# Kernel optimization log

Hardware: AMD Instinct MI355X
Metric: run time of the kernel (lower is better)

## Reference

```python
import jax, jax.numpy as jnp
import numpy as np

D = 1024      # n_embd
NH = 16       # attention heads
E = 8         # n_experts
K = 2         # k_best
FF = 4 * D    # expert MLP hidden
EPS = 1e-6    # rms_norm_epsilon
TEMP = 1.0    # target_temperature


def setup_inputs() -> dict:
    key = jax.random.key(0)
    ks = jax.random.split(key, 12)
    B, S = 2, 1024
    s = 0.02
    return {
        "x": jax.random.normal(ks[0], (B, S, D), jnp.float32),
        "attn_norm_w": jnp.ones((D,), jnp.float32),
        "wq": jax.random.normal(ks[1], (D, D), jnp.float32) * s,
        "wk": jax.random.normal(ks[2], (D, D), jnp.float32) * s,
        "wv": jax.random.normal(ks[3], (D, D), jnp.float32) * s,
        "wo": jax.random.normal(ks[4], (D, D), jnp.float32) * s,
        "mlp_norm_w": jnp.ones((D,), jnp.float32),
        "router_w": jax.random.normal(ks[5], (D, E), jnp.float32) * s,
        "w1": jax.random.normal(ks[6], (E, D, FF), jnp.float32) * s,
        "b1": jnp.zeros((E, FF), jnp.float32),
        "w2": jax.random.normal(ks[7], (E, FF, D), jnp.float32) * s,
        "b2": jnp.zeros((E, D), jnp.float32),
    }


def _rmsnorm(x, w):
    var = jnp.mean(jnp.square(x), axis=-1, keepdims=True)
    return x * jax.lax.rsqrt(var + EPS) * w


def _attention(x, wq, wk, wv, wo):
    B, S, _ = x.shape
    dh = D // NH
    q = (x @ wq).reshape(B, S, NH, dh)
    k = (x @ wk).reshape(B, S, NH, dh)
    v = (x @ wv).reshape(B, S, NH, dh)
    scores = jnp.einsum("bqhd,bkhd->bhqk", q, k) / jnp.sqrt(jnp.float32(dh))
    causal = jnp.tril(jnp.ones((S, S), bool))  # [S,S]
    scores = jnp.where(causal[None, None], scores, jnp.finfo(scores.dtype).min)
    attn = jax.nn.softmax(scores, axis=-1)
    out = jnp.einsum("bhqk,bkhd->bqhd", attn, v).reshape(B, S, D)
    return out @ wo


def reference(x, attn_norm_w, wq, wk, wv, wo, mlp_norm_w, router_w, w1, b1, w2, b2):
    B, S, _ = x.shape
    # attention sub-block
    x = x + _attention(_rmsnorm(x, attn_norm_w), wq, wk, wv, wo)
    residual = x
    h = _rmsnorm(x, mlp_norm_w)  # [B,S,D]

    # router: temperature softmax + top-k
    logits = h @ router_w / TEMP                      # [B,S,E]
    probs = jax.nn.softmax(logits, axis=-1)
    top_k_scores, top_k_indices = jax.lax.top_k(probs, K)  # [B,S,K]
    onehot = jax.nn.one_hot(top_k_indices, E, dtype=h.dtype)  # [B,S,K,E]
    gates = jnp.einsum("bsk,bske->bse", top_k_scores, onehot)  # [B,S,E]

    # load-balancing loss (Switch-style) + expert counts
    counts = jnp.sum(onehot, axis=(0, 1, 2))          # [E]
    frac = counts / (B * S * K)
    mean_prob = jnp.mean(probs, axis=(0, 1))          # [E]
    balancing_loss = E * jnp.sum(frac * mean_prob)

    # experts: dense dispatch; tokens with zero gate contribute nothing,
    # so this matches the sort/gather/scatter top-k combine exactly.
    pre = jnp.einsum("bsd,edf->ebsf", h, w1) + b1[:, None, None]  # [E,B,S,FF]
    act = jax.nn.gelu(pre)
    y = jnp.einsum("ebsf,efd->ebsd", act, w2) + b2[:, None, None]  # [E,B,S,D]
    moe = jnp.einsum("ebsd,bse->bsd", y, gates)

    out = residual + moe
    return out, balancing_loss, counts
```

## Files before the change

### kernel.cpp

```cpp
#include <hip/hip_runtime.h>

typedef __bf16 bf16;
typedef __bf16 bf16x8 __attribute__((ext_vector_type(8)));
typedef float f32x4 __attribute__((ext_vector_type(4)));

#define D_   1024
#define S_   1024
#define B_   2
#define NTOK 2048
#define FF_  4096
#define NE   8
#define CAP  5120
#define OUTN 2097152

__device__ __forceinline__ float gelu_f(float x) {
    return 0.5f * x * (1.0f + tanhf(0.7978845608028654f * (x + 0.044715f * x * x * x)));
}

__device__ __forceinline__ void gload16(const void* g, void* l) {
    __builtin_amdgcn_global_load_lds((const __attribute__((address_space(1))) unsigned int*)g,
                                     (__attribute__((address_space(3))) unsigned int*)l,
                                     16, 0, 0);
}

__global__ __launch_bounds__(256) void rmsnorm_k(const float* __restrict__ x,
                                                 const float* __restrict__ w,
                                                 float* __restrict__ yf,
                                                 bf16* __restrict__ yhi,
                                                 bf16* __restrict__ ylo) {
    int row = blockIdx.x;
    int t = threadIdx.x;
    const float* xr = x + (size_t)row * D_;
    float4 v = *(const float4*)(xr + t * 4);
    float ss = v.x * v.x + v.y * v.y + v.z * v.z + v.w * v.w;
    for (int off = 32; off; off >>= 1) ss += __shfl_down(ss, off);
    __shared__ float wsum[4];
    if ((t & 63) == 0) wsum[t >> 6] = ss;
    __syncthreads();
    float tot = wsum[0] + wsum[1] + wsum[2] + wsum[3];
    float rr = rsqrtf(tot * (1.0f / D_) + 1e-6f);
    float4 wv = *(const float4*)(w + t * 4);
    float y[4];
    y[0] = v.x * rr * wv.x; y[1] = v.y * rr * wv.y;
    y[2] = v.z * rr * wv.z; y[3] = v.w * rr * wv.w;
    if (yf) *(float4*)(yf + (size_t)row * D_ + t * 4) = *(float4*)y;
    if (yhi) {
#pragma unroll
        for (int i = 0; i < 4; i++) {
            bf16 hi = (bf16)y[i];
            yhi[(size_t)row * D_ + t * 4 + i] = hi;
            if (ylo) ylo[(size_t)row * D_ + t * 4 + i] = (bf16)(y[i] - (float)hi);
        }
    }
}

__global__ __launch_bounds__(256) void trans_split_k(
    const float* __restrict__ w0, const float* __restrict__ w1p,
    const float* __restrict__ w2p, const float* __restrict__ w3,
    bf16* o0h, bf16* o0l, bf16* o1h, bf16* o1l,
    bf16* o2h, bf16* o2l, bf16* o3h, bf16* o3l) {
    int z = blockIdx.z;
    const float* src = (z == 0) ? w0 : (z == 1) ? w1p : (z == 2) ? w2p : w3;
    bf16* dh = (z == 0) ? o0h : (z == 1) ? o1h : (z == 2) ? o2h : o3h;
    bf16* dl = (z == 0) ? o0l : (z == 1) ? o1l : (z == 2) ? o2l : o3l;
    __shared__ float tl[32][33];
    int c0 = blockIdx.x * 32, r0 = blockIdx.y * 32;
    int tx = threadIdx.x & 31, ty = threadIdx.x >> 5;
#pragma unroll
    for (int i = 0; i < 4; i++) {
        int r = ty + i * 8;
        tl[r][tx] = src[(size_t)(r0 + r) * 1024 + c0 + tx];
    }
    __syncthreads();
#pragma unroll
    for (int i = 0; i < 4; i++) {
        int c = ty + i * 8;
        float v = tl[tx][c];
        bf16 hi = (bf16)v;
        dh[(size_t)(c0 + c) * 1024 + r0 + tx] = hi;
        dl[(size_t)(c0 + c) * 1024 + r0 + tx] = (bf16)(v - (float)hi);
    }
}

__global__ __launch_bounds__(256) void transpose_cast_k(const float* __restrict__ in,
                                                        bf16* __restrict__ out,
                                                        int R, int C) {
    __shared__ float tl[32][33];
    size_t base = (size_t)blockIdx.z * R * C;
    const float* src = in + base;
    bf16* dst = out + base;
    int c0 = blockIdx.x * 32, r0 = blockIdx.y * 32;
    int tx = threadIdx.x & 31, tyy = threadIdx.x >> 5;
#pragma unroll
    for (int i = 0; i < 4; i++) {
        int r = tyy + i * 8;
        tl[r][tx] = src[(size_t)(r0 + r) * C + c0 + tx];
    }
    __syncthreads();
#pragma unroll
    for (int i = 0; i < 4; i++) {
        int c = tyy + i * 8;
        dst[(size_t)(c0 + c) * R + r0 + tx] = (bf16)tl[tx][c];
    }
}

#define GLD 40

#define GEMM64_SPLIT_BODY(N0EXPR, EPILOGUE)                                            \
    __shared__ bf16 Ash[64 * GLD], Asl[64 * GLD], Bsh[64 * GLD], Bsl[64 * GLD];        \
    int t = threadIdx.x;                                                               \
    int m0 = blockIdx.x * 64;                                                          \
    int n0 = (N0EXPR);                                                                 \
    int wv = t >> 6, ln = t & 63, l15 = ln & 15, qd = ln >> 4;                         \
    int srow = t >> 2, skc = (t & 3) * 8;                                              \
    f32x4 acc[4];                                                                      \
    _Pragma("unroll") for (int mt = 0; mt < 4; mt++) acc[mt] = (f32x4){0.f,0.f,0.f,0.f}; \
    for (int k0 = 0; k0 < 1024; k0 += 32) {                                            \
        __syncthreads();                                                               \
        *(bf16x8*)&Ash[srow * GLD + skc] = *(const bf16x8*)(Ah + (size_t)(m0 + srow) * 1024 + k0 + skc); \
        *(bf16x8*)&Asl[srow * GLD + skc] = *(const bf16x8*)(Al + (size_t)(m0 + srow) * 1024 + k0 + skc); \
        *(bf16x8*)&Bsh[srow * GLD + skc] = *(const bf16x8*)(Bh + (size_t)(n0 + srow) * 1024 + k0 + skc); \
        *(bf16x8*)&Bsl[srow * GLD + skc] = *(const bf16x8*)(Bl + (size_t)(n0 + srow) * 1024 + k0 + skc); \
        __syncthreads();                                                               \
        bf16x8 ah[4], al[4];                                                           \
        _Pragma("unroll") for (int mt = 0; mt < 4; mt++) {                             \
            ah[mt] = *(const bf16x8*)&Ash[(mt * 16 + l15) * GLD + qd * 8];             \
            al[mt] = *(const bf16x8*)&Asl[(mt * 16 + l15) * GLD + qd * 8];             \
        }                                                                              \
        bf16x8 bh = *(const bf16x8*)&Bsh[(wv * 16 + l15) * GLD + qd * 8];              \
        bf16x8 bl = *(const bf16x8*)&Bsl[(wv * 16 + l15) * GLD + qd * 8];              \
        _Pragma("unroll") for (int mt = 0; mt < 4; mt++) {                             \
            acc[mt] = __builtin_amdgcn_mfma_f32_16x16x32_bf16(ah[mt], bh, acc[mt], 0, 0, 0); \
            acc[mt] = __builtin_amdgcn_mfma_f32_16x16x32_bf16(ah[mt], bl, acc[mt], 0, 0, 0); \
            acc[mt] = __builtin_amdgcn_mfma_f32_16x16x32_bf16(al[mt], bh, acc[mt], 0, 0, 0); \
        }                                                                              \
    }                                                                                  \
    int gnl = wv * 16 + l15;                                                           \
    _Pragma("unroll") for (int mt = 0; mt < 4; mt++)                                   \
        _Pragma("unroll") for (int r = 0; r < 4; r++) {                                \
            int gm = m0 + mt * 16 + qd * 4 + r;                                        \
            float vv = acc[mt][r];                                                     \
            EPILOGUE                                                                   \
        }

__global__ __launch_bounds__(256) void gemm_qkv_k(
    const bf16* __restrict__ Ah, const bf16* __restrict__ Al,
    const bf16* __restrict__ Bqh, const bf16* __restrict__ Bql,
    const bf16* __restrict__ Bkh, const bf16* __restrict__ Bkl,
    const bf16* __restrict__ Bvh, const bf16* __restrict__ Bvl,
    bf16* Cqh, bf16* Cql, bf16* Ckh, bf16* Ckl, bf16* Cvh, bf16* Cvl) {
    int gy = blockIdx.y, zw = gy >> 4;
    const bf16* Bh = (zw == 0) ? Bqh : (zw == 1) ? Bkh : Bvh;
    const bf16* Bl = (zw == 0) ? Bql : (zw == 1) ? Bkl : Bvl;
    bf16* Ch = (zw == 0) ? Cqh : (zw == 1) ? Ckh : Cvh;
    bf16* Cl = (zw == 0) ? Cql : (zw == 1) ? Ckl : Cvl;
    GEMM64_SPLIT_BODY((gy & 15) * 64, {
        bf16 hi = (bf16)vv;
        Ch[(size_t)gm * D_ + n0 + gnl] = hi;
        Cl[(size_t)gm * D_ + n0 + gnl] = (bf16)(vv - (float)hi);
    })
}

__global__ __launch_bounds__(256) void gemm_wo_k(
    const bf16* __restrict__ Ah, const bf16* __restrict__ Al,
    const bf16* __restrict__ Bh, const bf16* __restrict__ Bl,
    float* __restrict__ C, const float* __restrict__ X) {
    GEMM64_SPLIT_BODY(blockIdx.y * 64, {
        C[(size_t)gm * D_ + n0 + gnl] = X[(size_t)gm * D_ + n0 + gnl] + vv;
    })
}

#define AP 72

__global__ __launch_bounds__(256) void attn_mfma_k(
    const bf16* __restrict__ qhp, const bf16* __restrict__ qlp,
    const bf16* __restrict__ khp, const bf16* __restrict__ klp,
    const bf16* __restrict__ vhp, const bf16* __restrict__ vlp,
    bf16* __restrict__ aoh, bf16* __restrict__ aol) {
    int qt = (int)gridDim.x - 1 - (int)blockIdx.x;
    int h = blockIdx.y, b = blockIdx.z;
    __shared__ bf16 Ksh[64 * AP], Ksl[64 * AP], VTh[64 * AP], VTl[64 * AP];
    __shared__ bf16 Ph[4][16 * AP], Pl[4][16 * AP];
    int t = threadIdx.x, wv = t >> 6, ln = t & 63, l15 = ln & 15, qd = ln >> 4;

    bf16x8 aqh[2], aql[2];
    {
        size_t qb = ((size_t)(b * S_ + qt * 64 + wv * 16 + l15)) * D_ + h * 64 + qd * 8;
        aqh[0] = *(const bf16x8*)(qhp + qb);
        aqh[1] = *(const bf16x8*)(qhp + qb + 32);
        aql[0] = *(const bf16x8*)(qlp + qb);
        aql[1] = *(const bf16x8*)(qlp + qb + 32);
    }
    f32x4 oacc[4];
    float mrow[4], lrow[4];
#pragma unroll
    for (int i = 0; i < 4; i++) {
        oacc[i] = (f32x4){0.f, 0.f, 0.f, 0.f};
        mrow[i] = -1e30f; lrow[i] = 0.0f;
    }

    for (int kt = 0; kt <= qt; kt++) {
        __syncthreads();
#pragma unroll
        for (int j = 0; j < 2; j++) {
            int idx = t + j * 256;
            int row = idx >> 3, ch = (idx & 7) * 8;
            size_t g = ((size_t)(b * S_ + kt * 64 + row)) * D_ + h * 64 + ch;
            *(bf16x8*)&Ksh[row * AP + ch] = *(const bf16x8*)(khp + g);
            *(bf16x8*)&Ksl[row * AP + ch] = *(const bf16x8*)(klp + g);
            bf16x8 vvh = *(const bf16x8*)(vhp + g);
            bf16x8 vvl = *(const bf16x8*)(vlp + g);
#pragma unroll
            for (int jj = 0; jj < 8; jj++) {
                VTh[(ch + jj) * AP + row] = vvh[jj];
                VTl[(ch + jj) * AP + row] = vvl[jj];
            }
        }
        __syncthreads();

        f32x4 sacc[4];
#pragma unroll
        for (int nt = 0; nt < 4; nt++) sacc[nt] = (f32x4){0.f, 0.f, 0.f, 0.f};
#pragma unroll
        for (int ks = 0; ks < 2; ks++) {
#pragma unroll
            for (int nt = 0; nt < 4; nt++) {
                bf16x8 bh = *(const bf16x8*)&Ksh[(nt * 16 + l15) * AP + ks * 32 + qd * 8];
                bf16x8 bl = *(const bf16x8*)&Ksl[(nt * 16 + l15) * AP + ks * 32 + qd * 8];
                sacc[nt] = __builtin_amdgcn_mfma_f32_16x16x32_bf16(aqh[ks], bh, sacc[nt], 0, 0, 0);
                sacc[nt] = __builtin_amdgcn_mfma_f32_16x16x32_bf16(aqh[ks], bl, sacc[nt], 0, 0, 0);
                sacc[nt] = __builtin_amdgcn_mfma_f32_16x16x32_bf16(aql[ks], bh, sacc[nt], 0, 0, 0);
            }
        }
        bool diag = (kt == qt);
#pragma unroll
        for (int r = 0; r < 4; r++) {
            float s0[4];
#pragma unroll
            for (int nt = 0; nt < 4; nt++) {
                s0[nt] = sacc[nt][r] * 0.125f;
                if (diag && (nt * 16 + l15) > (wv * 16 + qd * 4 + r)) s0[nt] = -1e30f;
            }
            float vmax = fmaxf(fmaxf(s0[0], s0[1]), fmaxf(s0[2], s0[3]));
            for (int off = 1; off < 16; off <<= 1) vmax = fmaxf(vmax, __shfl_xor(vmax, off));
            float mnew = fmaxf(mrow[r], vmax);
            float alpha = expf(mrow[r] - mnew);
            float p[4], rs = 0.0f;
#pragma unroll
            for (int nt = 0; nt < 4; nt++) { p[nt] = expf(s0[nt] - mnew); rs += p[nt]; }
            for (int off = 1; off < 16; off <<= 1) rs += __shfl_xor(rs, off);
            lrow[r] = lrow[r] * alpha + rs;
            mrow[r] = mnew;
#pragma unroll
            for (int nt = 0; nt < 4; nt++) oacc[nt][r] *= alpha;
            int prow = qd * 4 + r;
#pragma unroll
            for (int nt = 0; nt < 4; nt++) {
                bf16 hi = (bf16)p[nt];
                Ph[wv][prow * AP + nt * 16 + l15] = hi;
                Pl[wv][prow * AP + nt * 16 + l15] = (bf16)(p[nt] - (float)hi);
            }
        }
#pragma unroll
        for (int ks2 = 0; ks2 < 2; ks2++) {
            bf16x8 aph = *(const bf16x8*)&Ph[wv][l15 * AP + ks2 * 32 + qd * 8];
            bf16x8 apl = *(const bf16x8*)&Pl[wv][l15 * AP + ks2 * 32 + qd * 8];
#pragma unroll
            for (int nt = 0; nt < 4; nt++) {
                bf16x8 bvh = *(const bf16x8*)&VTh[(nt * 16 + l15) * AP + ks2 * 32 + qd * 8];
                bf16x8 bvl = *(const bf16x8*)&VTl[(nt * 16 + l15) * AP + ks2 * 32 + qd * 8];
                oacc[nt] = __builtin_amdgcn_mfma_f32_16x16x32_bf16(aph, bvh, oacc[nt], 0, 0, 0);
                oacc[nt] = __builtin_amdgcn_mfma_f32_16x16x32_bf16(aph, bvl, oacc[nt], 0, 0, 0);
                oacc[nt] = __builtin_amdgcn_mfma_f32_16x16x32_bf16(apl, bvh, oacc[nt], 0, 0, 0);
            }
        }
    }

#pragma unroll
    for (int r = 0; r < 4; r++) {
        float inv = 1.0f / lrow[r];
        size_t rowa = ((size_t)(b * S_ + qt * 64 + wv * 16 + qd * 4 + r)) * D_ + h * 64;
#pragma unroll
        for (int nt = 0; nt < 4; nt++) {
            float o = oacc[nt][r] * inv;
            bf16 hi = (bf16)o;
            aoh[rowa + nt * 16 + l15] = hi;
            aol[rowa + nt * 16 + l15] = (bf16)(o - (float)hi);
        }
    }
}

__global__ __launch_bounds__(256) void router_k(const float* __restrict__ h,
                                                const float* __restrict__ rw,
                                                int* __restrict__ tidx,
                                                float* __restrict__ tgate,
                                                int* __restrict__ ecnt,
                                                float* __restrict__ psum) {
    int wv = threadIdx.x >> 6, ln = threadIdx.x & 63;
    int tok = blockIdx.x * 4 + wv;
    const float* hr = h + (size_t)tok * D_;
    float acc[NE];
#pragma unroll
    for (int e = 0; e < NE; e++) acc[e] = 0.0f;
    int base = ln * 16;
#pragma unroll
    for (int c = 0; c < 4; c++) {
        float4 hv = *(const float4*)(hr + base + c * 4);
        const float* rp = rw + (size_t)(base + c * 4) * NE;
        float hx[4] = {hv.x, hv.y, hv.z, hv.w};
#pragma unroll
        for (int jj = 0; jj < 4; jj++)
#pragma unroll
            for (int e = 0; e < NE; e++)
                acc[e] = fmaf(hx[jj], rp[jj * NE + e], acc[e]);
    }
#pragma unroll
    for (int e = 0; e < NE; e++)
        for (int off = 32; off; off >>= 1) acc[e] += __shfl_down(acc[e], off);

    __shared__ float pb[4][NE];
    if (ln == 0) {
        float mx = acc[0];
#pragma unroll
        for (int e = 1; e < NE; e++) mx = fmaxf(mx, acc[e]);
        float p[NE], ssum = 0.0f;
#pragma unroll
        for (int e = 0; e < NE; e++) { p[e] = expf(acc[e] - mx); ssum += p[e]; }
        float inv = 1.0f / ssum;
#pragma unroll
        for (int e = 0; e < NE; e++) p[e] *= inv;
        int i0 = 0; float b0 = p[0];
#pragma unroll
        for (int e = 1; e < NE; e++) if (p[e] > b0) { b0 = p[e]; i0 = e; }
        int i1 = -1; float b1v = -1.0f;
#pragma unroll
        for (int e = 0; e < NE; e++) if (e != i0 && p[e] > b1v) { b1v = p[e]; i1 = e; }
        tidx[tok * 2] = i0; tidx[tok * 2 + 1] = i1;
        tgate[tok * 2] = b0; tgate[tok * 2 + 1] = b1v;
        atomicAdd(&ecnt[i0], 1);
        atomicAdd(&ecnt[i1], 1);
#pragma unroll
        for (int e = 0; e < NE; e++) pb[wv][e] = p[e];
    }
    __syncthreads();
    if (threadIdx.x < NE) {
        float s2 = pb[0][threadIdx.x] + pb[1][threadIdx.x] + pb[2][threadIdx.x] + pb[3][threadIdx.x];
        atomicAdd(&psum[threadIdx.x], s2);
    }
}

__global__ void passb_k(const int* __restrict__ ecnt, const float* __restrict__ psum,
                        int* __restrict__ eoffp, int* __restrict__ ecnt2,
                        float* __restrict__ out_tail) {
    if (threadIdx.x == 0) {
        int off = 0; float loss = 0.0f;
        for (int e = 0; e < NE; e++) {
            eoffp[e] = off;
            int c = ecnt[e];
            off += (c + 127) & ~127;
            loss += (c * (1.0f / 4096.0f)) * (psum[e] * (1.0f / 2048.0f));
            out_tail[1 + e] = (float)c;
            ecnt2[e] = 0;
        }
        eoffp[NE] = off;
        out_tail[0] = 8.0f * loss;
    }
}

__global__ __launch_bounds__(256) void scatter_k(const int* __restrict__ tidx,
                                                 const int* __restrict__ eoffp,
                                                 int* __restrict__ ecnt2,
                                                 int* __restrict__ stok,
                                                 int* __restrict__ sidx) {
    int tok = blockIdx.x * 256 + threadIdx.x;
    for (int k = 0; k < 2; k++) {
        int e = tidx[tok * 2 + k];
        int pos = eoffp[e] + atomicAdd(&ecnt2[e], 1);
        stok[pos] = tok;
        sidx[tok * 2 + k] = pos;
    }
}

__global__ __launch_bounds__(256) void moe_gemm1_k(const bf16* __restrict__ hB,
                                                   const bf16* __restrict__ w1t,
                                                   const float* __restrict__ b1,
                                                   const int* __restrict__ eoffp,
                                                   const int* __restrict__ stok,
                                                   bf16* __restrict__ act) {
    int m0 = blockIdx.x * 128, n0 = blockIdx.y * 128;
    if (m0 >= eoffp[NE]) return;
    int e = 0;
#pragma unroll
    for (int i = 1; i < NE; i++) if (m0 >= eoffp[i]) e = i;

    __shared__ __align__(16) bf16 As[128 * 32];
    __shared__ __align__(16) bf16 Bs[128 * 32];
    int t = threadIdx.x;
    int wv = t >> 6, ln = t & 63;
    int wm = wv >> 1, wn = wv & 1, l15 = ln & 15, qd = ln >> 4;

    int sr0 = t >> 2, sr1 = 64 + sr0, cl = t & 3;
    int cs0 = (cl ^ ((sr0 >> 1) & 3)) * 8;
    int cs1 = (cl ^ ((sr1 >> 1) & 3)) * 8;
    const bf16* ga0 = hB + (size_t)stok[m0 + sr0] * D_ + cs0;
    const bf16* ga1 = hB + (size_t)stok[m0 + sr1] * D_ + cs1;
    const bf16* Bb = w1t + ((size_t)e * FF_ + n0) * D_;
    const bf16* gb0 = Bb + (size_t)sr0 * D_ + cs0;
    const bf16* gb1 = Bb + (size_t)sr1 * D_ + cs1;
    bf16* lA0 = As + wv * 512;  bf16* lA1 = As + 2048 + wv * 512;
    bf16* lB0 = Bs + wv * 512;  bf16* lB1 = Bs + 2048 + wv * 512;

    const bf16 *ra[4], *rb[4];
#pragma unroll
    for (int i = 0; i < 4; i++) {
        int r1 = wm * 64 + i * 16 + l15;
        ra[i] = As + r1 * 32 + (qd ^ ((r1 >> 1) & 3)) * 8;
        int r2 = wn * 64 + i * 16 + l15;
        rb[i] = Bs + r2 * 32 + (qd ^ ((r2 >> 1) & 3)) * 8;
    }

    f32x4 acc[4][4];
#pragma unroll
    for (int mt = 0; mt < 4; mt++)
#pragma unroll
        for (int nt = 0; nt < 4; nt++) acc[mt][nt] = (f32x4){0.f, 0.f, 0.f, 0.f};

    for (int k0 = 0; k0 < D_; k0 += 32) {
        __syncthreads();
        gload16(ga0 + k0, lA0);
        gload16(ga1 + k0, lA1);
        gload16(gb0 + k0, lB0);
        gload16(gb1 + k0, lB1);
        __syncthreads();
        bf16x8 af[4], bfr[4];
#pragma unroll
        for (int i = 0; i < 4; i++) {
            af[i] = *(const bf16x8*)ra[i];
            bfr[i] = *(const bf16x8*)rb[i];
        }
#pragma unroll
        for (int mt = 0; mt < 4; mt++)
#pragma unroll
            for (int nt = 0; nt < 4; nt++)
                acc[mt][nt] = __builtin_amdgcn_mfma_f32_16x16x32_bf16(af[mt], bfr[nt], acc[mt][nt], 0, 0, 0);
    }

    const float* b1e = b1 + (size_t)e * FF_;
#pragma unroll
    for (int mt = 0; mt < 4; mt++)
#pragma unroll
        for (int nt = 0; nt < 4; nt++) {
            int gn = n0 + wn * 64 + nt * 16 + l15;
            float bias = b1e[gn];
#pragma unroll
            for (int r = 0; r < 4; r++) {
                int gm = m0 + wm * 64 + mt * 16 + qd * 4 + r;
                act[(size_t)gm * FF_ + gn] = (bf16)gelu_f(acc[mt][nt][r] + bias);
            }
        }
}

__global__ __launch_bounds__(256) void moe_gemm2_k(const bf16* __restrict__ act,
                                                   const bf16* __restrict__ w2t,
                                                   const float* __restrict__ b2,
                                                   const int* __restrict__ eoffp,
                                                   float* __restrict__ y) {
    int m0 = blockIdx.x * 128, n0 = blockIdx.y * 128;
    if (m0 >= eoffp[NE]) return;
    int e = 0;
#pragma unroll
    for (int i = 1; i < NE; i++) if (m0 >= eoffp[i]) e = i;

    __shared__ __align__(16) bf16 As[128 * 32];
    __shared__ __align__(16) bf16 Bs[128 * 32];
    int t = threadIdx.x;
    int wv = t >> 6, ln = t & 63;
    int wm = wv >> 1, wn = wv & 1, l15 = ln & 15, qd = ln >> 4;

    int sr0 = t >> 2, sr1 = 64 + sr0, cl = t & 3;
    int cs0 = (cl ^ ((sr0 >> 1) & 3)) * 8;
    int cs1 = (cl ^ ((sr1 >> 1) & 3)) * 8;
    const bf16* ga0 = act + (size_t)(m0 + sr0) * FF_ + cs0;
    const bf16* ga1 = act + (size_t)(m0 + sr1) * FF_ + cs1;
    const bf16* Bb = w2t + ((size_t)e * D_ + n0) * FF_;
    const bf16* gb0 = Bb + (size_t)sr0 * FF_ + cs0;
    const bf16* gb1 = Bb + (size_t)sr1 * FF_ + cs1;
    bf16* lA0 = As + wv * 512;  bf16* lA1 = As + 2048 + wv * 512;
    bf16* lB0 = Bs + wv * 512;  bf16* lB1 = Bs + 2048 + wv * 512;

    const bf16 *ra[4], *rb[4];
#pragma unroll
    for (int i = 0; i < 4; i++) {
        int r1 = wm * 64 + i * 16 + l15;
        ra[i] = As + r1 * 32 + (qd ^ ((r1 >> 1) & 3)) * 8;
        int r2 = wn * 64 + i * 16 + l15;
        rb[i] = Bs + r2 * 32 + (qd ^ ((r2 >> 1) & 3)) * 8;
    }

    f32x4 acc[4][4];
#pragma unroll
    for (int mt = 0; mt < 4; mt++)
#pragma unroll
        for (int nt = 0; nt < 4; nt++) acc[mt][nt] = (f32x4){0.f, 0.f, 0.f, 0.f};

    for (int k0 = 0; k0 < FF_; k0 += 32) {
        __syncthreads();
        gload16(ga0 + k0, lA0);
        gload16(ga1 + k0, lA1);
        gload16(gb0 + k0, lB0);
        gload16(gb1 + k0, lB1);
        __syncthreads();
        bf16x8 af[4], bfr[4];
#pragma unroll
        for (int i = 0; i < 4; i++) {
            af[i] = *(const bf16x8*)ra[i];
            bfr[i] = *(const bf16x8*)rb[i];
        }
#pragma unroll
        for (int mt = 0; mt < 4; mt++)
#pragma unroll
            for (int nt = 0; nt < 4; nt++)
                acc[mt][nt] = __builtin_amdgcn_mfma_f32_16x16x32_bf16(af[mt], bfr[nt], acc[mt][nt], 0, 0, 0);
    }

    const float* b2e = b2 + (size_t)e * D_;
#pragma unroll
    for (int mt = 0; mt < 4; mt++)
#pragma unroll
        for (int nt = 0; nt < 4; nt++) {
            int gn = n0 + wn * 64 + nt * 16 + l15;
            float bias = b2e[gn];
#pragma unroll
            for (int r = 0; r < 4; r++) {
                int gm = m0 + wm * 64 + mt * 16 + qd * 4 + r;
                y[(size_t)gm * D_ + gn] = acc[mt][nt][r] + bias;
            }
        }
}

__global__ __launch_bounds__(256) void combine_k(const float* __restrict__ y,
                                                 const int* __restrict__ sidx,
                                                 const float* __restrict__ tgate,
                                                 float* __restrict__ out) {
    int tok = blockIdx.x;
    int d = threadIdx.x * 4;
    int s0 = sidx[tok * 2], s1 = sidx[tok * 2 + 1];
    float g0 = tgate[tok * 2], g1 = tgate[tok * 2 + 1];
    float4 a = *(const float4*)(y + (size_t)s0 * D_ + d);
    float4 b = *(const float4*)(y + (size_t)s1 * D_ + d);
    float4 o = *(const float4*)(out + (size_t)tok * D_ + d);
    o.x += g0 * a.x + g1 * b.x;
    o.y += g0 * a.y + g1 * b.y;
    o.z += g0 * a.z + g1 * b.z;
    o.w += g0 * a.w + g1 * b.w;
    *(float4*)(out + (size_t)tok * D_ + d) = o;
}

extern "C" void kernel_launch(void* const* d_in, const int* in_sizes, int n_in,
                              void* d_out, int out_size, void* d_ws, size_t ws_size,
                              hipStream_t stream) {
    const float* x   = (const float*)d_in[0];
    const float* anw = (const float*)d_in[1];
    const float* wq  = (const float*)d_in[2];
    const float* wk  = (const float*)d_in[3];
    const float* wv  = (const float*)d_in[4];
    const float* wo  = (const float*)d_in[5];
    const float* mnw = (const float*)d_in[6];
    const float* rw  = (const float*)d_in[7];
    const float* w1  = (const float*)d_in[8];
    const float* b1  = (const float*)d_in[9];
    const float* w2  = (const float*)d_in[10];
    const float* b2  = (const float*)d_in[11];
    float* out = (float*)d_out;

    char* p = (char*)d_ws;
    auto take = [&](size_t n) { char* r = p; p += (n + 255) & ~(size_t)255; return r; };
    bf16* h1h = (bf16*)take((size_t)OUTN * 2);
    bf16* h1l = (bf16*)take((size_t)OUTN * 2);
    bf16* qh  = (bf16*)take((size_t)OUTN * 2);
    bf16* ql  = (bf16*)take((size_t)OUTN * 2);
    bf16* kh  = (bf16*)take((size_t)OUTN * 2);
    bf16* kl  = (bf16*)take((size_t)OUTN * 2);
    bf16* vh  = (bf16*)take((size_t)OUTN * 2);
    bf16* vl  = (bf16*)take((size_t)OUTN * 2);
    bf16* wqth = (bf16*)take((size_t)D_ * D_ * 2);
    bf16* wqtl = (bf16*)take((size_t)D_ * D_ * 2);
    bf16* wkth = (bf16*)take((size_t)D_ * D_ * 2);
    bf16* wktl = (bf16*)take((size_t)D_ * D_ * 2);
    bf16* wvth = (bf16*)take((size_t)D_ * D_ * 2);
    bf16* wvtl = (bf16*)take((size_t)D_ * D_ * 2);
    bf16* woth = (bf16*)take((size_t)D_ * D_ * 2);
    bf16* wotl = (bf16*)take((size_t)D_ * D_ * 2);
    bf16* w1t = (bf16*)take((size_t)NE * FF_ * D_ * 2);
    bf16* w2t = (bf16*)take((size_t)NE * FF_ * D_ * 2);
    bf16* act = (bf16*)take((size_t)CAP * FF_ * 2);
    int*   tidx  = (int*)take(NTOK * 2 * 4);
    float* tgate = (float*)take(NTOK * 2 * 4);
    int*   sidx  = (int*)take(NTOK * 2 * 4);
    int*   ecnt  = (int*)take(64);
    int*   ecnt2 = (int*)take(64);
    float* psum  = (float*)take(64);
    int*   eoffp = (int*)take(64);
    int*   stok  = (int*)take(CAP * 4);

    bf16*  aoh = h1h;
    bf16*  aol = h1l;
    float* h_f = (float*)qh;
    bf16*  h_b = kh;
    float* y   = (float*)vh;

    hipMemsetAsync(ecnt, 0, NE * 4, stream);
    hipMemsetAsync(psum, 0, NE * 4, stream);
    hipMemsetAsync(stok, 0, CAP * 4, stream);

    trans_split_k<<<dim3(32, 32, 4), 256, 0, stream>>>(wq, wk, wv, wo,
        wqth, wqtl, wkth, wktl, wvth, wvtl, woth, wotl);
    transpose_cast_k<<<dim3(FF_ / 32, D_ / 32, NE), 256, 0, stream>>>(w1, w1t, D_, FF_);
    transpose_cast_k<<<dim3(D_ / 32, FF_ / 32, NE), 256, 0, stream>>>(w2, w2t, FF_, D_);

    rmsnorm_k<<<NTOK, 256, 0, stream>>>(x, anw, nullptr, h1h, h1l);
    gemm_qkv_k<<<dim3(32, 48), 256, 0, stream>>>(h1h, h1l,
        wqth, wqtl, wkth, wktl, wvth, wvtl, qh, ql, kh, kl, vh, vl);
    attn_mfma_k<<<dim3(16, 16, 2), 256, 0, stream>>>(qh, ql, kh, kl, vh, vl, aoh, aol);
    gemm_wo_k<<<dim3(32, 16), 256, 0, stream>>>(aoh, aol, woth, wotl, out, x);

    rmsnorm_k<<<NTOK, 256, 0, stream>>>(out, mnw, h_f, h_b, nullptr);
    router_k<<<NTOK / 4, 256, 0, stream>>>(h_f, rw, tidx, tgate, ecnt, psum);
    passb_k<<<1, 64, 0, stream>>>(ecnt, psum, eoffp, ecnt2, out + OUTN);
    scatter_k<<<NTOK / 256, 256, 0, stream>>>(tidx, eoffp, ecnt2, stok, sidx);
    moe_gemm1_k<<<dim3(CAP / 128, FF_ / 128), 256, 0, stream>>>(h_b, w1t, b1, eoffp, stok, act);
    moe_gemm2_k<<<dim3(CAP / 128, D_ / 128), 256, 0, stream>>>(act, w2t, b2, eoffp, y);
    combine_k<<<NTOK, 256, 0, stream>>>(y, sidx, tgate, out);
}
```

Before: 787.2 us.

## Double-buffer LDS in MoE GEMMs and retile split-precision attention GEMMs to 128x128

The two MoE expert GEMMs now keep two LDS buffers and issue the async global-to-LDS loads for the next k-slice before running MFMAs on the current one, so memory latency overlaps with compute. The QKV and output-projection split-bf16 GEMMs move from 64x64 tiles with register loads to 128x128 tiles that use the same swizzled, double-buffered async-load pipeline. This raises arithmetic intensity per tile. The cost is fewer blocks for the small projection GEMMs (128 and 384) and more LDS per block (64 KB for the split GEMMs), which may limit occupancy.

```diff
diff --git a/kernel.cpp b/kernel.cpp
--- a/kernel.cpp
+++ b/kernel.cpp
@@ -104,42 +104,76 @@
     }
 }
 
-#define GLD 40
-
-#define GEMM64_SPLIT_BODY(N0EXPR, EPILOGUE)                                            \
-    __shared__ bf16 Ash[64 * GLD], Asl[64 * GLD], Bsh[64 * GLD], Bsl[64 * GLD];        \
+#define SPLIT_STAGE(bi, k0)                             \
+    gload16(gah0 + (k0), Lah[bi] + wv * 512);           \
+    gload16(gah1 + (k0), Lah[bi] + 2048 + wv * 512);    \
+    gload16(gal0 + (k0), Lal[bi] + wv * 512);           \
+    gload16(gal1 + (k0), Lal[bi] + 2048 + wv * 512);    \
+    gload16(gbh0 + (k0), Lbh[bi] + wv * 512);           \
+    gload16(gbh1 + (k0), Lbh[bi] + 2048 + wv * 512);    \
+    gload16(gbl0 + (k0), Lbl[bi] + wv * 512);           \
+    gload16(gbl1 + (k0), Lbl[bi] + 2048 + wv * 512);
+
+#define SPLIT_COMPUTE(bi) {                                                            \
+    bf16x8 fah[4], fal[4], fbh[4], fbl[4];                                             \
+    _Pragma("unroll") for (int i = 0; i < 4; i++) {                                    \
+        fah[i] = *(const bf16x8*)(Lah[bi] + ra_off[i]);                                \
+        fal[i] = *(const bf16x8*)(Lal[bi] + ra_off[i]);                                \
+        fbh[i] = *(const bf16x8*)(Lbh[bi] + rb_off[i]);                                \
+        fbl[i] = *(const bf16x8*)(Lbl[bi] + rb_off[i]);                                \
+    }                                                                                  \
+    _Pragma("unroll") for (int mt = 0; mt < 4; mt++)                                   \
+    _Pragma("unroll") for (int nt = 0; nt < 4; nt++) {                                 \
+        acc[mt][nt] = __builtin_amdgcn_mfma_f32_16x16x32_bf16(fah[mt], fbh[nt], acc[mt][nt], 0, 0, 0); \
+        acc[mt][nt] = __builtin_amdgcn_mfma_f32_16x16x32_bf16(fah[mt], fbl[nt], acc[mt][nt], 0, 0, 0); \
+        acc[mt][nt] = __builtin_amdgcn_mfma_f32_16x16x32_bf16(fal[mt], fbh[nt], acc[mt][nt], 0, 0, 0); \
+    } }
+
+#define GEMM128_SPLIT_BODY(EPILOGUE)                                                   \
+    __shared__ __align__(16) bf16 Lah[2][4096];                                        \
+    __shared__ __align__(16) bf16 Lal[2][4096];                                        \
+    __shared__ __align__(16) bf16 Lbh[2][4096];                                        \
+    __shared__ __align__(16) bf16 Lbl[2][4096];                                        \
     int t = threadIdx.x;                                                               \
-    int m0 = blockIdx.x * 64;                                                          \
-    int n0 = (N0EXPR);                                                                 \
-    int wv = t >> 6, ln = t & 63, l15 = ln & 15, qd = ln >> 4;                         \
-    int srow = t >> 2, skc = (t & 3) * 8;                                              \
-    f32x4 acc[4];                                                                      \
-    _Pragma("unroll") for (int mt = 0; mt < 4; mt++) acc[mt] = (f32x4){0.f,0.f,0.f,0.f}; \
-    for (int k0 = 0; k0 < 1024; k0 += 32) {                                            \
+    int wv = t >> 6, ln = t & 63;                                                      \
+    int wm = wv >> 1, wn = wv & 1, l15 = ln & 15, qd = ln >> 4;                        \
+    int sr0 = t >> 2, sr1 = 64 + sr0, cl = t & 3;                                      \
+    int cs0 = (cl ^ ((sr0 >> 1) & 3)) * 8;                                             \
+    int cs1 = (cl ^ ((sr1 >> 1) & 3)) * 8;                                             \
+    const bf16* gah0 = Ah + (size_t)(m0 + sr0) * 1024 + cs0;                           \
+    const bf16* gah1 = Ah + (size_t)(m0 + sr1) * 1024 + cs1;                           \
+    const bf16* gal0 = Al + (size_t)(m0 + sr0) * 1024 + cs0;                           \
+    const bf16* gal1 = Al + (size_t)(m0 + sr1) * 1024 + cs1;                           \
+    const bf16* gbh0 = Bh + (size_t)(n0 + sr0) * 1024 + cs0;                           \
+    const bf16* gbh1 = Bh + (size_t)(n0 + sr1) * 1024 + cs1;                           \
+    const bf16* gbl0 = Bl + (size_t)(n0 + sr0) * 1024 + cs0;                           \
+    const bf16* gbl1 = Bl + (size_t)(n0 + sr1) * 1024 + cs1;                           \
+    int ra_off[4], rb_off[4];                                                          \
+    _Pragma("unroll") for (int i = 0; i < 4; i++) {                                    \
+        int r1 = wm * 64 + i * 16 + l15;                                               \
+        ra_off[i] = r1 * 32 + (qd ^ ((r1 >> 1) & 3)) * 8;                              \
+        int r2 = wn * 64 + i * 16 + l15;                                               \
+        rb_off[i] = r2 * 32 + (qd ^ ((r2 >> 1) & 3)) * 8;                              \
+    }                                                                                  \
+    f32x4 acc[4][4];                                                                   \
+    _Pragma("unroll") for (int mt = 0; mt < 4; mt++)                                   \
+    _Pragma("unroll") for (int nt = 0; nt < 4; nt++) acc[mt][nt] = (f32x4){0.f,0.f,0.f,0.f}; \
+    SPLIT_STAGE(0, 0);                                                                 \
+    __syncthreads();                                                                   \
+    for (int k0 = 0; k0 < 1024; k0 += 64) {                                            \
+        SPLIT_STAGE(1, k0 + 32);                                                       \
+        SPLIT_COMPUTE(0);                                                              \
         __syncthreads();                                                               \
-        *(bf16x8*)&Ash[srow * GLD + skc] = *(const bf16x8*)(Ah + (size_t)(m0 + srow) * 1024 + k0 + skc); \
-        *(bf16x8*)&Asl[srow * GLD + skc] = *(const bf16x8*)(Al + (size_t)(m0 + srow) * 1024 + k0 + skc); \
-        *(bf16x8*)&Bsh[srow * GLD + skc] = *(const bf16x8*)(Bh + (size_t)(n0 + srow) * 1024 + k0 + skc); \
-        *(bf16x8*)&Bsl[srow * GLD + skc] = *(const bf16x8*)(Bl + (size_t)(n0 + srow) * 1024 + k0 + skc); \
+        if (k0 + 64 < 1024) { SPLIT_STAGE(0, k0 + 64); }                               \
+        SPLIT_COMPUTE(1);                                                              \
         __syncthreads();                                                               \
-        bf16x8 ah[4], al[4];                                                           \
-        _Pragma("unroll") for (int mt = 0; mt < 4; mt++) {                             \
-            ah[mt] = *(const bf16x8*)&Ash[(mt * 16 + l15) * GLD + qd * 8];             \
-            al[mt] = *(const bf16x8*)&Asl[(mt * 16 + l15) * GLD + qd * 8];             \
-        }                                                                              \
-        bf16x8 bh = *(const bf16x8*)&Bsh[(wv * 16 + l15) * GLD + qd * 8];              \
-        bf16x8 bl = *(const bf16x8*)&Bsl[(wv * 16 + l15) * GLD + qd * 8];              \
-        _Pragma("unroll") for (int mt = 0; mt < 4; mt++) {                             \
-            acc[mt] = __builtin_amdgcn_mfma_f32_16x16x32_bf16(ah[mt], bh, acc[mt], 0, 0, 0); \
-            acc[mt] = __builtin_amdgcn_mfma_f32_16x16x32_bf16(ah[mt], bl, acc[mt], 0, 0, 0); \
-            acc[mt] = __builtin_amdgcn_mfma_f32_16x16x32_bf16(al[mt], bh, acc[mt], 0, 0, 0); \
-        }                                                                              \
     }                                                                                  \
-    int gnl = wv * 16 + l15;                                                           \
     _Pragma("unroll") for (int mt = 0; mt < 4; mt++)                                   \
+    _Pragma("unroll") for (int nt = 0; nt < 4; nt++)                                   \
         _Pragma("unroll") for (int r = 0; r < 4; r++) {                                \
-            int gm = m0 + mt * 16 + qd * 4 + r;                                        \
-            float vv = acc[mt][r];                                                     \
+            int gm = m0 + wm * 64 + mt * 16 + qd * 4 + r;                              \
+            int gn = n0 + wn * 64 + nt * 16 + l15;                                     \
+            float vv = acc[mt][nt][r];                                                 \
             EPILOGUE                                                                   \
         }
 
@@ -149,15 +183,16 @@
     const bf16* __restrict__ Bkh, const bf16* __restrict__ Bkl,
     const bf16* __restrict__ Bvh, const bf16* __restrict__ Bvl,
     bf16* Cqh, bf16* Cql, bf16* Ckh, bf16* Ckl, bf16* Cvh, bf16* Cvl) {
-    int gy = blockIdx.y, zw = gy >> 4;
+    int gy = blockIdx.y, zw = gy >> 3;
     const bf16* Bh = (zw == 0) ? Bqh : (zw == 1) ? Bkh : Bvh;
     const bf16* Bl = (zw == 0) ? Bql : (zw == 1) ? Bkl : Bvl;
     bf16* Ch = (zw == 0) ? Cqh : (zw == 1) ? Ckh : Cvh;
     bf16* Cl = (zw == 0) ? Cql : (zw == 1) ? Ckl : Cvl;
-    GEMM64_SPLIT_BODY((gy & 15) * 64, {
+    int m0 = blockIdx.x * 128, n0 = (gy & 7) * 128;
+    GEMM128_SPLIT_BODY({
         bf16 hi = (bf16)vv;
-        Ch[(size_t)gm * D_ + n0 + gnl] = hi;
-        Cl[(size_t)gm * D_ + n0 + gnl] = (bf16)(vv - (float)hi);
+        Ch[(size_t)gm * D_ + gn] = hi;
+        Cl[(size_t)gm * D_ + gn] = (bf16)(vv - (float)hi);
     })
 }
 
@@ -165,8 +200,9 @@
     const bf16* __restrict__ Ah, const bf16* __restrict__ Al,
     const bf16* __restrict__ Bh, const bf16* __restrict__ Bl,
     float* __restrict__ C, const float* __restrict__ X) {
-    GEMM64_SPLIT_BODY(blockIdx.y * 64, {
-        C[(size_t)gm * D_ + n0 + gnl] = X[(size_t)gm * D_ + n0 + gnl] + vv;
+    int m0 = blockIdx.x * 128, n0 = blockIdx.y * 128;
+    GEMM128_SPLIT_BODY({
+        C[(size_t)gm * D_ + gn] = X[(size_t)gm * D_ + gn] + vv;
     })
 }
 
@@ -381,6 +417,22 @@
     }
 }
 
+#define MOE_STAGE(bufA, bufB, k0)                       \
+    gload16(ga0 + (k0), bufA + wv * 512);               \
+    gload16(ga1 + (k0), bufA + 2048 + wv * 512);        \
+    gload16(gb0 + (k0), bufB + wv * 512);               \
+    gload16(gb1 + (k0), bufB + 2048 + wv * 512);
+
+#define MOE_COMPUTE(bufA, bufB) {                                                      \
+    bf16x8 af[4], bfr[4];                                                              \
+    _Pragma("unroll") for (int i = 0; i < 4; i++) {                                    \
+        af[i]  = *(const bf16x8*)(bufA + ra_off[i]);                                   \
+        bfr[i] = *(const bf16x8*)(bufB + rb_off[i]);                                   \
+    }                                                                                  \
+    _Pragma("unroll") for (int mt = 0; mt < 4; mt++)                                   \
+    _Pragma("unroll") for (int nt = 0; nt < 4; nt++)                                   \
+        acc[mt][nt] = __builtin_amdgcn_mfma_f32_16x16x32_bf16(af[mt], bfr[nt], acc[mt][nt], 0, 0, 0); }
+
 __global__ __launch_bounds__(256) void moe_gemm1_k(const bf16* __restrict__ hB,
                                                    const bf16* __restrict__ w1t,
                                                    const float* __restrict__ b1,
@@ -393,8 +445,8 @@
 #pragma unroll
     for (int i = 1; i < NE; i++) if (m0 >= eoffp[i]) e = i;
 
-    __shared__ __align__(16) bf16 As[128 * 32];
-    __shared__ __align__(16) bf16 Bs[128 * 32];
+    __shared__ __align__(16) bf16 As[2][4096];
+    __shared__ __align__(16) bf16 Bs[2][4096];
     int t = threadIdx.x;
     int wv = t >> 6, ln = t & 63;
     int wm = wv >> 1, wn = wv & 1, l15 = ln & 15, qd = ln >> 4;
@@ -407,16 +459,14 @@
     const bf16* Bb = w1t + ((size_t)e * FF_ + n0) * D_;
     const bf16* gb0 = Bb + (size_t)sr0 * D_ + cs0;
     const bf16* gb1 = Bb + (size_t)sr1 * D_ + cs1;
-    bf16* lA0 = As + wv * 512;  bf16* lA1 = As + 2048 + wv * 512;
-    bf16* lB0 = Bs + wv * 512;  bf16* lB1 = Bs + 2048 + wv * 512;
-
-    const bf16 *ra[4], *rb[4];
+
+    int ra_off[4], rb_off[4];
 #pragma unroll
     for (int i = 0; i < 4; i++) {
         int r1 = wm * 64 + i * 16 + l15;
-        ra[i] = As + r1 * 32 + (qd ^ ((r1 >> 1) & 3)) * 8;
+        ra_off[i] = r1 * 32 + (qd ^ ((r1 >> 1) & 3)) * 8;
         int r2 = wn * 64 + i * 16 + l15;
-        rb[i] = Bs + r2 * 32 + (qd ^ ((r2 >> 1) & 3)) * 8;
+        rb_off[i] = r2 * 32 + (qd ^ ((r2 >> 1) & 3)) * 8;
     }
 
     f32x4 acc[4][4];
@@ -425,24 +475,15 @@
 #pragma unroll
         for (int nt = 0; nt < 4; nt++) acc[mt][nt] = (f32x4){0.f, 0.f, 0.f, 0.f};
 
-    for (int k0 = 0; k0 < D_; k0 += 32) {
+    MOE_STAGE(As[0], Bs[0], 0);
+    __syncthreads();
+    for (int k0 = 0; k0 < D_; k0 += 64) {
+        MOE_STAGE(As[1], Bs[1], k0 + 32);
+        MOE_COMPUTE(As[0], Bs[0]);
         __syncthreads();
-        gload16(ga0 + k0, lA0);
-        gload16(ga1 + k0, lA1);
-        gload16(gb0 + k0, lB0);
-        gload16(gb1 + k0, lB1);
+        if (k0 + 64 < D_) { MOE_STAGE(As[0], Bs[0], k0 + 64); }
+        MOE_COMPUTE(As[1], Bs[1]);
         __syncthreads();
-        bf16x8 af[4], bfr[4];
-#pragma unroll
-        for (int i = 0; i < 4; i++) {
-            af[i] = *(const bf16x8*)ra[i];
-            bfr[i] = *(const bf16x8*)rb[i];
-        }
-#pragma unroll
-        for (int mt = 0; mt < 4; mt++)
-#pragma unroll
-            for (int nt = 0; nt < 4; nt++)
-                acc[mt][nt] = __builtin_amdgcn_mfma_f32_16x16x32_bf16(af[mt], bfr[nt], acc[mt][nt], 0, 0, 0);
     }
 
     const float* b1e = b1 + (size_t)e * FF_;
@@ -471,8 +512,8 @@
 #pragma unroll
     for (int i = 1; i < NE; i++) if (m0 >= eoffp[i]) e = i;
 
-    __shared__ __align__(16) bf16 As[128 * 32];
-    __shared__ __align__(16) bf16 Bs[128 * 32];
+    __shared__ __align__(16) bf16 As[2][4096];
+    __shared__ __align__(16) bf16 Bs[2][4096];
     int t = threadIdx.x;
     int wv = t >> 6, ln = t & 63;
     int wm = wv >> 1, wn = wv & 1, l15 = ln & 15, qd = ln >> 4;
@@ -485,16 +526,14 @@
     const bf16* Bb = w2t + ((size_t)e * D_ + n0) * FF_;
     const bf16* gb0 = Bb + (size_t)sr0 * FF_ + cs0;
     const bf16* gb1 = Bb + (size_t)sr1 * FF_ + cs1;
-    bf16* lA0 = As + wv * 512;  bf16* lA1 = As + 2048 + wv * 512;
-    bf16* lB0 = Bs + wv * 512;  bf16* lB1 = Bs + 2048 + wv * 512;
-
-    const bf16 *ra[4], *rb[4];
+
+    int ra_off[4], rb_off[4];
 #pragma unroll
     for (int i = 0; i < 4; i++) {
         int r1 = wm * 64 + i * 16 + l15;
-        ra[i] = As + r1 * 32 + (qd ^ ((r1 >> 1) & 3)) * 8;
+        ra_off[i] = r1 * 32 + (qd ^ ((r1 >> 1) & 3)) * 8;
         int r2 = wn * 64 + i * 16 + l15;
-        rb[i] = Bs + r2 * 32 + (qd ^ ((r2 >> 1) & 3)) * 8;
+        rb_off[i] = r2 * 32 + (qd ^ ((r2 >> 1) & 3)) * 8;
     }
 
     f32x4 acc[4][4];
@@ -503,24 +542,15 @@
 #pragma unroll
         for (int nt = 0; nt < 4; nt++) acc[mt][nt] = (f32x4){0.f, 0.f, 0.f, 0.f};
 
-    for (int k0 = 0; k0 < FF_; k0 += 32) {
+    MOE_STAGE(As[0], Bs[0], 0);
+    __syncthreads();
+    for (int k0 = 0; k0 < FF_; k0 += 64) {
+        MOE_STAGE(As[1], Bs[1], k0 + 32);
+        MOE_COMPUTE(As[0], Bs[0]);
         __syncthreads();
-        gload16(ga0 + k0, lA0);
-        gload16(ga1 + k0, lA1);
-        gload16(gb0 + k0, lB0);
-        gload16(gb1 + k0, lB1);
+        if (k0 + 64 < FF_) { MOE_STAGE(As[0], Bs[0], k0 + 64); }
+        MOE_COMPUTE(As[1], Bs[1]);
         __syncthreads();
-        bf16x8 af[4], bfr[4];
-#pragma unroll
-        for (int i = 0; i < 4; i++) {
-            af[i] = *(const bf16x8*)ra[i];
-            bfr[i] = *(const bf16x8*)rb[i];
-        }
-#pragma unroll
-        for (int mt = 0; mt < 4; mt++)
-#pragma unroll
-            for (int nt = 0; nt < 4; nt++)
-                acc[mt][nt] = __builtin_amdgcn_mfma_f32_16x16x32_bf16(af[mt], bfr[nt], acc[mt][nt], 0, 0, 0);
     }
 
     const float* b2e = b2 + (size_t)e * D_;
@@ -619,10 +649,10 @@
     transpose_cast_k<<<dim3(D_ / 32, FF_ / 32, NE), 256, 0, stream>>>(w2, w2t, FF_, D_);
 
     rmsnorm_k<<<NTOK, 256, 0, stream>>>(x, anw, nullptr, h1h, h1l);
-    gemm_qkv_k<<<dim3(32, 48), 256, 0, stream>>>(h1h, h1l,
+    gemm_qkv_k<<<dim3(16, 24), 256, 0, stream>>>(h1h, h1l,
         wqth, wqtl, wkth, wktl, wvth, wvtl, qh, ql, kh, kl, vh, vl);
     attn_mfma_k<<<dim3(16, 16, 2), 256, 0, stream>>>(qh, ql, kh, kl, vh, vl, aoh, aol);
-    gemm_wo_k<<<dim3(32, 16), 256, 0, stream>>>(aoh, aol, woth, wotl, out, x);
+    gemm_wo_k<<<dim3(16, 8), 256, 0, stream>>>(aoh, aol, woth, wotl, out, x);
 
     rmsnorm_k<<<NTOK, 256, 0, stream>>>(out, mnw, h_f, h_b, nullptr);
     router_k<<<NTOK / 4, 256, 0, stream>>>(h_f, rw, tidx, tgate, ecnt, psum);
```

Measured after the change: 805.1 us. 1.02x slower.
